# Kernel optimization log

Measured on AMD Instinct MI355X. Metric: run time of the kernel, lower is better.

## Reference

```python
import jax, jax.numpy as jnp
import numpy as np

CTX = 5  # context_len

def z_vector(x, ctx):
    # x: [B, L, E] -> [B, L, ctx*E]; slot j holds embedding of token (idx + j - ctx//2), zero-padded at edges
    half = ctx // 2
    B, L, E = x.shape
    xp = jnp.pad(x, ((0, 0), (half, half), (0, 0)))
    return jnp.concatenate([xp[:, i:i + L, :] for i in range(ctx)], axis=-1)

def setup_inputs() -> dict:
    key = jax.random.key(0)
    kq, ka, kw, kb = jax.random.split(key, 4)
    B, LQ, LA, E, F = 256, 64, 256, 300, 512
    question = jax.random.normal(kq, (B, LQ, E), dtype=jnp.float32)
    answer = jax.random.normal(ka, (B, LA, E), dtype=jnp.float32)
    W = jax.random.normal(kw, (CTX * E, F), dtype=jnp.float32) * 0.02
    b = jax.random.normal(kb, (F,), dtype=jnp.float32) * 0.02
    return {"question": question, "answer": answer, "W": W, "b": b}

def reference(question, answer, W, b):
    # Conv2d(1, F, (ctx*E, 1)) over the full-height Z vector == per-position linear map
    def branch(x):
        z = z_vector(x, CTX)                       # [B, L, ctx*E]
        out = jnp.einsum('blk,kf->bfl', z, W)      # [B, F, L]
        return out + b[None, :, None]
    return branch(question), branch(answer)
```

## Files before the change

### kernel.cpp

```cpp
#include <hip/hip_runtime.h>

#define NB   256
#define E0   300
#define EP   304
#define F_   512
#define KP   1536
#define NKT  48
#define LQ_  64
#define LA_  256

typedef __attribute__((ext_vector_type(4))) float f32x4;
typedef __attribute__((ext_vector_type(8))) short short8;

#define XQ_ELEMS (NB * (LQ_ + 4) * EP)
#define XA_ELEMS (NB * (LA_ + 4) * EP)
#define WF_ELEMS (F_ * KP)
#define OUTQ_ELEMS ((size_t)NB * F_ * LQ_)
#define XROWS (NB * (LQ_ + 4) + NB * (LA_ + 4))

__device__ __forceinline__ unsigned short f2bf(float x) {
    unsigned int u = __float_as_uint(x);
    u = u + 0x7fffu + ((u >> 16) & 1u);
    return (unsigned short)(u >> 16);
}

__global__ void prep_x(const float* __restrict__ q, const float* __restrict__ a,
                       unsigned short* __restrict__ xq, unsigned short* __restrict__ xa)
{
    int idx = blockIdx.x * 256 + threadIdx.x;
    if (idx >= XROWS * 76) return;
    int row = idx / 76;
    int col = idx - row * 76;

    const float* src;
    unsigned short* dst;
    bool valid;
    if (row < NB * (LQ_ + 4)) {
        int b = row / (LQ_ + 4), lp = row - b * (LQ_ + 4);
        dst = xq + (size_t)row * EP;
        valid = (lp >= 2 && lp < 2 + LQ_);
        src = q + ((size_t)b * LQ_ + (lp - 2)) * E0;
    } else {
        int r2 = row - NB * (LQ_ + 4);
        int b = r2 / (LA_ + 4), lp = r2 - b * (LA_ + 4);
        dst = xa + (size_t)r2 * EP;
        valid = (lp >= 2 && lp < 2 + LA_);
        src = a + ((size_t)b * LA_ + (lp - 2)) * E0;
    }
    unsigned long long pk = 0ull;
    if (valid && col < 75) {
        const float4 v = reinterpret_cast<const float4*>(src)[col];
        pk = (unsigned long long)f2bf(v.x)
           | ((unsigned long long)f2bf(v.y) << 16)
           | ((unsigned long long)f2bf(v.z) << 32)
           | ((unsigned long long)f2bf(v.w) << 48);
    }
    *reinterpret_cast<unsigned long long*>(dst + (size_t)col * 4) = pk;
}

__global__ void prep_w2(const float* __restrict__ W, unsigned short* __restrict__ wfr)
{
    int idx = blockIdx.x * 256 + threadIdx.x;
    int j    = idx & 7;
    int lane = (idx >> 3) & 63;
    int chunk = idx >> 9;
    int kc = chunk % NKT;
    int tile16 = chunk / NKT;
    int f  = tile16 * 16 + (lane & 15);
    int kp = kc * 32 + (lane >> 4) * 8 + j;
    int jj = kp / EP;
    int e  = kp - jj * EP;
    float v = (kp < 5 * EP && e < E0) ? W[(size_t)(jj * E0 + e) * F_ + f] : 0.f;
    wfr[idx] = f2bf(v);
}

__global__ __launch_bounds__(256, 3) void qa_gemm(
    const unsigned short* __restrict__ xq,
    const unsigned short* __restrict__ xa,
    const unsigned short* __restrict__ wfr,
    const float* __restrict__ bias,
    float* __restrict__ out)
{
    __shared__ __align__(16) unsigned short lds[4 * 2048];

    const int bid = blockIdx.x;
    const int wg  = (bid & 7) * 320 + (bid >> 3);

    const unsigned short* xp;
    float* ob;
    int Mbase, lsh, Lp, ftBase;
    if (wg < 512) {
        Mbase  = (wg >> 1) * 64;
        ftBase = (wg & 1) * 256;
        xp = xq; lsh = 6; Lp = LQ_ + 4;
        ob = out;
    } else {
        const int id = wg - 512;
        Mbase  = (id >> 1) * 64;
        ftBase = (id & 1) * 256;
        xp = xa; lsh = 8; Lp = LA_ + 4;
        ob = out + OUTQ_ELEMS;
    }
    const int Lv = 1 << lsh;

    const int tid  = threadIdx.x;
    const int lane = tid & 63;
    const int wid  = tid >> 6;
    const int lq   = lane >> 4;
    const int lr   = lane & 15;

    const int s_c  = (lane & 3) ^ ((lane >> 3) & 3);
    const int sub  = lane >> 2;
    const int mr0 = Mbase + wid * 16 + sub;
    const unsigned short* gZ0 = xp + (size_t)((mr0 >> lsh) * Lp + (mr0 & (Lv - 1))) * EP + s_c * 8;
    const int dz0 = wid * 512;

#define GLLDS(p, d) __builtin_amdgcn_global_load_lds(                               \
        (const __attribute__((address_space(1))) void*)(p),                         \
        (__attribute__((address_space(3))) void*)(d), 16, 0, 0)
#define STAGE_Z(T) do { const int rb = ((T) & 3) * 2048; const size_t ko = (size_t)(T) * 32; \
    GLLDS(gZ0 + ko, lds + dz0 + rb); } while (0)

    const unsigned short* wpc0 = wfr + (size_t)((ftBase >> 4) + wid * 4 + 0) * NKT * 512 + lane * 8;
    const unsigned short* wpc1 = wfr + (size_t)((ftBase >> 4) + wid * 4 + 1) * NKT * 512 + lane * 8;
    const unsigned short* wpc2 = wfr + (size_t)((ftBase >> 4) + wid * 4 + 2) * NKT * 512 + lane * 8;
    const unsigned short* wpc3 = wfr + (size_t)((ftBase >> 4) + wid * 4 + 3) * NKT * 512 + lane * 8;

#define WLOAD(dst, p) do {                                                           \
    asm volatile("global_load_dwordx4 %0, %1, off" : "=v"(dst) : "v"(p) : "memory"); \
    (p) += 512; } while (0)

    const int cs = (lq ^ ((lr >> 1) & 3)) * 16;
    int zoff[4];
#pragma unroll
    for (int n = 0; n < 4; ++n) zoff[n] = (n * 16 + lr) * 64 + cs;

    f32x4 acc[4][4] = {};
    short8 WA0, WA1, WA2, WA3, WB0, WB1, WB2, WB3;

#define MFMA(a, b, c) __builtin_amdgcn_mfma_f32_16x16x32_bf16((a), (b), (c), 0, 0, 0)

#define KSTEP(T, C0, C1, C2, C3, N0, N1, N2, N3, DO_W, DO_Z, AV) do {               \
    const char* bb = (const char*)lds + ((T) & 3) * 4096;                           \
    short8 zf[4];                                                                   \
    _Pragma("unroll") for (int n = 0; n < 4; ++n) zf[n] = *(const short8*)(bb + zoff[n]); \
    if (DO_W) { WLOAD(N0, wpc0); WLOAD(N1, wpc1); WLOAD(N2, wpc2); WLOAD(N3, wpc3); } \
    if (DO_Z) { STAGE_Z((T) + 3); }                                                 \
    asm volatile("s_waitcnt vmcnt(" #AV ") lgkmcnt(0)" ::: "memory");               \
    __builtin_amdgcn_sched_barrier(0);                                              \
    _Pragma("unroll") for (int n = 0; n < 4; ++n) {                                 \
        acc[0][n] = MFMA(C0, zf[n], acc[0][n]);                                     \
        acc[1][n] = MFMA(C1, zf[n], acc[1][n]);                                     \
        acc[2][n] = MFMA(C2, zf[n], acc[2][n]);                                     \
        acc[3][n] = MFMA(C3, zf[n], acc[3][n]);                                     \
    }                                                                               \
    asm volatile("s_barrier" ::: "memory");                                         \
} while (0)

    WLOAD(WA0, wpc0); WLOAD(WA1, wpc1); WLOAD(WA2, wpc2); WLOAD(WA3, wpc3);
    STAGE_Z(0); STAGE_Z(1); STAGE_Z(2);
    asm volatile("s_waitcnt vmcnt(2)\n\ts_barrier" ::: "memory");

    for (int i = 0; i < 22; ++i) {
        const int t = 2 * i;
        KSTEP(t,     WA0, WA1, WA2, WA3, WB0, WB1, WB2, WB3, 1, 1, 6);
        KSTEP(t + 1, WB0, WB1, WB2, WB3, WA0, WA1, WA2, WA3, 1, 1, 6);
    }
    KSTEP(44, WA0, WA1, WA2, WA3, WB0, WB1, WB2, WB3, 1, 1, 6);
    KSTEP(45, WB0, WB1, WB2, WB3, WA0, WA1, WA2, WA3, 1, 0, 5);
    KSTEP(46, WA0, WA1, WA2, WA3, WB0, WB1, WB2, WB3, 1, 0, 4);
    KSTEP(47, WB0, WB1, WB2, WB3, WA0, WA1, WA2, WA3, 0, 0, 0);

#undef KSTEP
#undef WLOAD
#undef STAGE_Z
#undef GLLDS
#undef MFMA

#pragma unroll
    for (int ns = 0; ns < 4; ++ns) {
        const int m = Mbase + ns * 16 + lr;
        const int b = m >> lsh;
        const int l = m & (Lv - 1);
        float* orow = ob + ((size_t)b * F_ << lsh) + l;
#pragma unroll
        for (int ms = 0; ms < 4; ++ms) {
            const int f0 = ftBase + wid * 64 + ms * 16 + lq * 4;
            const f32x4 v = acc[ms][ns];
#pragma unroll
            for (int r = 0; r < 4; ++r)
                orow[(size_t)(f0 + r) << lsh] = v[r] + __ldg(&bias[f0 + r]);
        }
    }
}

extern "C" void kernel_launch(void* const* d_in, const int* in_sizes, int n_in,
                              void* d_out, int out_size, void* d_ws, size_t ws_size,
                              hipStream_t stream)
{
    const float* q    = (const float*)d_in[0];
    const float* a    = (const float*)d_in[1];
    const float* W    = (const float*)d_in[2];
    const float* bias = (const float*)d_in[3];
    float* out = (float*)d_out;

    unsigned short* xq  = (unsigned short*)d_ws;
    unsigned short* xa  = xq + XQ_ELEMS;
    unsigned short* wfr = xa + XA_ELEMS;

    prep_x<<<(XROWS * 76 + 255) / 256, 256, 0, stream>>>(q, a, xq, xa);
    prep_w2<<<WF_ELEMS / 256, 256, 0, stream>>>(W, wfr);
    qa_gemm<<<2560, 256, 0, stream>>>(xq, xa, wfr, bias, out);
}
```

Baseline: 169.0 us.

## Stage Z in 128-wide superstages with double buffering and register prefetch

Replaces the 4-deep per-k-step LDS ring (one barrier per 32-wide k-step) with a 2-buffer scheme. Each stage loads four k-steps of Z at once, so there is one barrier per 128 k. LDS fragments for the next sub-step are prefetched into registers while the MFMAs for the current one issue, and s_setprio raises wave priority around the MFMA blocks. The aim is fewer workgroup barriers and better overlap of LDS reads with matrix math. The cost is a doubled LDS footprint (32KB), which may reduce occupancy, and more registers.

```diff
diff --git a/kernel.cpp b/kernel.cpp
--- a/kernel.cpp
+++ b/kernel.cpp
@@ -6,6 +6,7 @@
 #define F_   512
 #define KP   1536
 #define NKT  48
+#define NSS  12
 #define LQ_  64
 #define LA_  256
 
@@ -81,7 +82,7 @@
     const float* __restrict__ bias,
     float* __restrict__ out)
 {
-    __shared__ __align__(16) unsigned short lds[4 * 2048];
+    __shared__ __align__(16) unsigned short lds[2 * 8192];
 
     const int bid = blockIdx.x;
     const int wg  = (bid & 7) * 320 + (bid >> 3);
@@ -118,8 +119,11 @@
 #define GLLDS(p, d) __builtin_amdgcn_global_load_lds(                               \
         (const __attribute__((address_space(1))) void*)(p),                         \
         (__attribute__((address_space(3))) void*)(d), 16, 0, 0)
-#define STAGE_Z(T) do { const int rb = ((T) & 3) * 2048; const size_t ko = (size_t)(T) * 32; \
-    GLLDS(gZ0 + ko, lds + dz0 + rb); } while (0)
+#define STAGE_SS(T) do { const int rb = ((T) & 1) * 8192; const size_t ko = (size_t)(T) * 128; \
+    GLLDS(gZ0 + ko +  0, lds + rb + 0 * 2048 + dz0);                                \
+    GLLDS(gZ0 + ko + 32, lds + rb + 1 * 2048 + dz0);                                \
+    GLLDS(gZ0 + ko + 64, lds + rb + 2 * 2048 + dz0);                                \
+    GLLDS(gZ0 + ko + 96, lds + rb + 3 * 2048 + dz0); } while (0)
 
     const unsigned short* wpc0 = wfr + (size_t)((ftBase >> 4) + wid * 4 + 0) * NKT * 512 + lane * 8;
     const unsigned short* wpc1 = wfr + (size_t)((ftBase >> 4) + wid * 4 + 1) * NKT * 512 + lane * 8;
@@ -136,44 +140,56 @@
     for (int n = 0; n < 4; ++n) zoff[n] = (n * 16 + lr) * 64 + cs;
 
     f32x4 acc[4][4] = {};
-    short8 WA0, WA1, WA2, WA3, WB0, WB1, WB2, WB3;
+    short8 zA[4], zB[4], wA[4], wB[4];
 
 #define MFMA(a, b, c) __builtin_amdgcn_mfma_f32_16x16x32_bf16((a), (b), (c), 0, 0, 0)
 
-#define KSTEP(T, C0, C1, C2, C3, N0, N1, N2, N3, DO_W, DO_Z, AV) do {               \
-    const char* bb = (const char*)lds + ((T) & 3) * 4096;                           \
-    short8 zf[4];                                                                   \
-    _Pragma("unroll") for (int n = 0; n < 4; ++n) zf[n] = *(const short8*)(bb + zoff[n]); \
-    if (DO_W) { WLOAD(N0, wpc0); WLOAD(N1, wpc1); WLOAD(N2, wpc2); WLOAD(N3, wpc3); } \
-    if (DO_Z) { STAGE_Z((T) + 3); }                                                 \
-    asm volatile("s_waitcnt vmcnt(" #AV ") lgkmcnt(0)" ::: "memory");               \
+#define KSUB(bb, NXT, ZU, ZL, WU, WL, DO_ZRD, DO_W, VMCV, LGKV) do {                \
+    if (DO_ZRD) { _Pragma("unroll") for (int n = 0; n < 4; ++n)                     \
+        ZL[n] = *(const short8*)((bb) + (NXT) * 4096 + zoff[n]); }                  \
+    if (DO_W) { WLOAD(WL[0], wpc0); WLOAD(WL[1], wpc1);                             \
+                WLOAD(WL[2], wpc2); WLOAD(WL[3], wpc3); }                           \
+    asm volatile("s_waitcnt vmcnt(" #VMCV ") lgkmcnt(" #LGKV ")" ::: "memory");     \
     __builtin_amdgcn_sched_barrier(0);                                              \
+    __builtin_amdgcn_s_setprio(1);                                                  \
     _Pragma("unroll") for (int n = 0; n < 4; ++n) {                                 \
-        acc[0][n] = MFMA(C0, zf[n], acc[0][n]);                                     \
-        acc[1][n] = MFMA(C1, zf[n], acc[1][n]);                                     \
-        acc[2][n] = MFMA(C2, zf[n], acc[2][n]);                                     \
-        acc[3][n] = MFMA(C3, zf[n], acc[3][n]);                                     \
+        acc[0][n] = MFMA(WU[0], ZU[n], acc[0][n]);                                  \
+        acc[1][n] = MFMA(WU[1], ZU[n], acc[1][n]);                                  \
+        acc[2][n] = MFMA(WU[2], ZU[n], acc[2][n]);                                  \
+        acc[3][n] = MFMA(WU[3], ZU[n], acc[3][n]);                                  \
     }                                                                               \
-    asm volatile("s_barrier" ::: "memory");                                         \
+    __builtin_amdgcn_s_setprio(0);                                                  \
+    __builtin_amdgcn_sched_barrier(0);                                              \
 } while (0)
 
-    WLOAD(WA0, wpc0); WLOAD(WA1, wpc1); WLOAD(WA2, wpc2); WLOAD(WA3, wpc3);
-    STAGE_Z(0); STAGE_Z(1); STAGE_Z(2);
-    asm volatile("s_waitcnt vmcnt(2)\n\ts_barrier" ::: "memory");
-
-    for (int i = 0; i < 22; ++i) {
-        const int t = 2 * i;
-        KSTEP(t,     WA0, WA1, WA2, WA3, WB0, WB1, WB2, WB3, 1, 1, 6);
-        KSTEP(t + 1, WB0, WB1, WB2, WB3, WA0, WA1, WA2, WA3, 1, 1, 6);
-    }
-    KSTEP(44, WA0, WA1, WA2, WA3, WB0, WB1, WB2, WB3, 1, 1, 6);
-    KSTEP(45, WB0, WB1, WB2, WB3, WA0, WA1, WA2, WA3, 1, 0, 5);
-    KSTEP(46, WA0, WA1, WA2, WA3, WB0, WB1, WB2, WB3, 1, 0, 4);
-    KSTEP(47, WB0, WB1, WB2, WB3, WA0, WA1, WA2, WA3, 0, 0, 0);
-
-#undef KSTEP
+    WLOAD(wA[0], wpc0); WLOAD(wA[1], wpc1); WLOAD(wA[2], wpc2); WLOAD(wA[3], wpc3);
+    STAGE_SS(0);
+    asm volatile("s_waitcnt vmcnt(0)\n\ts_barrier" ::: "memory");
+
+    for (int S = 0; S < 11; ++S) {
+        const char* bb = (const char*)lds + (S & 1) * 16384;
+#pragma unroll
+        for (int n = 0; n < 4; ++n) zA[n] = *(const short8*)(bb + zoff[n]);
+        STAGE_SS(S + 1);
+        KSUB(bb, 1, zA, zB, wA, wB, 1, 1, 8, 4);
+        KSUB(bb, 2, zB, zA, wB, wA, 1, 1, 4, 4);
+        KSUB(bb, 3, zA, zB, wA, wB, 1, 1, 4, 4);
+        KSUB(bb, 0, zB, zA, wB, wA, 0, 1, 4, 0);
+        asm volatile("s_barrier" ::: "memory");
+    }
+    {
+        const char* bb = (const char*)lds + (11 & 1) * 16384;
+#pragma unroll
+        for (int n = 0; n < 4; ++n) zA[n] = *(const short8*)(bb + zoff[n]);
+        KSUB(bb, 1, zA, zB, wA, wB, 1, 1, 4, 4);
+        KSUB(bb, 2, zB, zA, wB, wA, 1, 1, 4, 4);
+        KSUB(bb, 3, zA, zB, wA, wB, 1, 1, 4, 4);
+        KSUB(bb, 0, zB, zA, wB, wA, 0, 0, 0, 0);
+    }
+
+#undef KSUB
 #undef WLOAD
-#undef STAGE_Z
+#undef STAGE_SS
 #undef GLLDS
 #undef MFMA
 
```

Result: faster. 164.1 us (-2.9%).

## Restructure GEMM pipeline into 4-step superstages with triple-buffered W registers

Applied to the files above, without the earlier changes.

Replaces the per-K-step LDS ring (4 slots of one 32-wide K chunk each, one barrier per step) with 3 LDS superstage buffers holding four K chunks each. This cuts workgroup barriers to one per four K steps, and the W fragments move to a three-deep register rotation. MFMA bursts are wrapped in s_setprio to favour matrix issue. LDS use grows from 16KB to 48KB per block, which may limit occupancy under launch_bounds(256,3), and the hand-tuned vmcnt values must exactly match the load order.

```diff
diff --git a/kernel.cpp b/kernel.cpp
--- a/kernel.cpp
+++ b/kernel.cpp
@@ -81,7 +81,7 @@
     const float* __restrict__ bias,
     float* __restrict__ out)
 {
-    __shared__ __align__(16) unsigned short lds[4 * 2048];
+    __shared__ __align__(16) unsigned short lds[3 * 8192];
 
     const int bid = blockIdx.x;
     const int wg  = (bid & 7) * 320 + (bid >> 3);
@@ -118,8 +118,11 @@
 #define GLLDS(p, d) __builtin_amdgcn_global_load_lds(                               \
         (const __attribute__((address_space(1))) void*)(p),                         \
         (__attribute__((address_space(3))) void*)(d), 16, 0, 0)
-#define STAGE_Z(T) do { const int rb = ((T) & 3) * 2048; const size_t ko = (size_t)(T) * 32; \
-    GLLDS(gZ0 + ko, lds + dz0 + rb); } while (0)
+#define STAGE_SS(T, RB3) do { const int rb = (RB3) * 8192; const size_t ko = (size_t)(T) * 128; \
+    GLLDS(gZ0 + ko +  0, lds + rb + 0 * 2048 + dz0);                                \
+    GLLDS(gZ0 + ko + 32, lds + rb + 1 * 2048 + dz0);                                \
+    GLLDS(gZ0 + ko + 64, lds + rb + 2 * 2048 + dz0);                                \
+    GLLDS(gZ0 + ko + 96, lds + rb + 3 * 2048 + dz0); } while (0)
 
     const unsigned short* wpc0 = wfr + (size_t)((ftBase >> 4) + wid * 4 + 0) * NKT * 512 + lane * 8;
     const unsigned short* wpc1 = wfr + (size_t)((ftBase >> 4) + wid * 4 + 1) * NKT * 512 + lane * 8;
@@ -129,6 +132,8 @@
 #define WLOAD(dst, p) do {                                                           \
     asm volatile("global_load_dwordx4 %0, %1, off" : "=v"(dst) : "v"(p) : "memory"); \
     (p) += 512; } while (0)
+#define WLD4(G) do { WLOAD(G[0], wpc0); WLOAD(G[1], wpc1);                           \
+                     WLOAD(G[2], wpc2); WLOAD(G[3], wpc3); } while (0)
 
     const int cs = (lq ^ ((lr >> 1) & 3)) * 16;
     int zoff[4];
@@ -136,44 +141,60 @@
     for (int n = 0; n < 4; ++n) zoff[n] = (n * 16 + lr) * 64 + cs;
 
     f32x4 acc[4][4] = {};
-    short8 WA0, WA1, WA2, WA3, WB0, WB1, WB2, WB3;
+    short8 w0[4], w1[4], w2[4];
 
 #define MFMA(a, b, c) __builtin_amdgcn_mfma_f32_16x16x32_bf16((a), (b), (c), 0, 0, 0)
 
-#define KSTEP(T, C0, C1, C2, C3, N0, N1, N2, N3, DO_W, DO_Z, AV) do {               \
-    const char* bb = (const char*)lds + ((T) & 3) * 4096;                           \
-    short8 zf[4];                                                                   \
-    _Pragma("unroll") for (int n = 0; n < 4; ++n) zf[n] = *(const short8*)(bb + zoff[n]); \
-    if (DO_W) { WLOAD(N0, wpc0); WLOAD(N1, wpc1); WLOAD(N2, wpc2); WLOAD(N3, wpc3); } \
-    if (DO_Z) { STAGE_Z((T) + 3); }                                                 \
-    asm volatile("s_waitcnt vmcnt(" #AV ") lgkmcnt(0)" ::: "memory");               \
-    __builtin_amdgcn_sched_barrier(0);                                              \
-    _Pragma("unroll") for (int n = 0; n < 4; ++n) {                                 \
-        acc[0][n] = MFMA(C0, zf[n], acc[0][n]);                                     \
-        acc[1][n] = MFMA(C1, zf[n], acc[1][n]);                                     \
-        acc[2][n] = MFMA(C2, zf[n], acc[2][n]);                                     \
-        acc[3][n] = MFMA(C3, zf[n], acc[3][n]);                                     \
-    }                                                                               \
-    asm volatile("s_barrier" ::: "memory");                                         \
-} while (0)
-
-    WLOAD(WA0, wpc0); WLOAD(WA1, wpc1); WLOAD(WA2, wpc2); WLOAD(WA3, wpc3);
-    STAGE_Z(0); STAGE_Z(1); STAGE_Z(2);
-    asm volatile("s_waitcnt vmcnt(2)\n\ts_barrier" ::: "memory");
-
-    for (int i = 0; i < 22; ++i) {
-        const int t = 2 * i;
-        KSTEP(t,     WA0, WA1, WA2, WA3, WB0, WB1, WB2, WB3, 1, 1, 6);
-        KSTEP(t + 1, WB0, WB1, WB2, WB3, WA0, WA1, WA2, WA3, 1, 1, 6);
-    }
-    KSTEP(44, WA0, WA1, WA2, WA3, WB0, WB1, WB2, WB3, 1, 1, 6);
-    KSTEP(45, WB0, WB1, WB2, WB3, WA0, WA1, WA2, WA3, 1, 0, 5);
-    KSTEP(46, WA0, WA1, WA2, WA3, WB0, WB1, WB2, WB3, 1, 0, 4);
-    KSTEP(47, WB0, WB1, WB2, WB3, WA0, WA1, WA2, WA3, 0, 0, 0);
-
-#undef KSTEP
+#define FENCE(VM, LG) do {                                                           \
+    asm volatile("s_waitcnt vmcnt(" #VM ") lgkmcnt(" #LG ")" ::: "memory");          \
+    __builtin_amdgcn_sched_barrier(0); } while (0)
+
+#define MFMA16(WU, ZU) do {                                                          \
+    __builtin_amdgcn_s_setprio(1);                                                   \
+    _Pragma("unroll") for (int n = 0; n < 4; ++n) {                                  \
+        acc[0][n] = MFMA(WU[0], ZU[n], acc[0][n]);                                   \
+        acc[1][n] = MFMA(WU[1], ZU[n], acc[1][n]);                                   \
+        acc[2][n] = MFMA(WU[2], ZU[n], acc[2][n]);                                   \
+        acc[3][n] = MFMA(WU[3], ZU[n], acc[3][n]);                                   \
+    }                                                                                \
+    __builtin_amdgcn_s_setprio(0);                                                   \
+    __builtin_amdgcn_sched_barrier(0); } while (0)
+
+#define ZRD(DST, BLK) do { _Pragma("unroll") for (int n = 0; n < 4; ++n)             \
+    DST[n] = *(const short8*)(bb + (BLK) * 4096 + zoff[n]); } while (0)
+
+#define SSBODY(P, WA_, WB_, WC_, DO_ST, STT, STB, DW2, DW3, V0, V1, V2, V3)          \
+{   const char* bb = (const char*)lds + (P) * 16384;                                 \
+    short8 zA[4], zB[4];                                                             \
+    ZRD(zA, 0);                                                                      \
+     ZRD(zB, 1); WLD4(WC_);                  FENCE(V0, 4); MFMA16(WA_, zA); \
+     ZRD(zA, 2); WLD4(WA_);                  FENCE(V1, 4); MFMA16(WB_, zB); \
+     ZRD(zB, 3); if (DW2) { WLD4(WB_); }                                    \
+              if (DO_ST) { STAGE_SS(STT, STB); }      FENCE(V2, 4); MFMA16(WC_, zA); \
+     if (DW3) { WLD4(WC_); }                 FENCE(V3, 0); MFMA16(WA_, zB); \
+    asm volatile("s_barrier" ::: "memory");                                          \
+}
+
+    WLD4(w0); WLD4(w1);
+    STAGE_SS(0, 0); STAGE_SS(1, 1);
+    asm volatile("s_waitcnt vmcnt(0)\n\ts_barrier" ::: "memory");
+
+    for (int Sb = 0; Sb < 9; Sb += 3) {
+        SSBODY(0, w0, w1, w2, 1, Sb + 2, 2, 1, 1, 12, 8, 12, 12);
+        SSBODY(1, w1, w2, w0, 1, Sb + 3, 0, 1, 1, 12, 8, 12, 12);
+        SSBODY(2, w2, w0, w1, 1, Sb + 4, 1, 1, 1, 12, 8, 12, 12);
+    }
+    SSBODY(0, w0, w1, w2, 1, 11, 2, 1, 1, 12, 8, 12, 12);
+    SSBODY(1, w1, w2, w0, 0, 0, 0, 1, 1, 12, 8, 8, 8);
+    SSBODY(2, w2, w0, w1, 0, 0, 0, 0, 0, 8, 8, 4, 0);
+
+#undef SSBODY
+#undef ZRD
+#undef MFMA16
+#undef FENCE
+#undef WLD4
 #undef WLOAD
-#undef STAGE_Z
+#undef STAGE_SS
 #undef GLLDS
 #undef MFMA
 
```

New measurement: 162.4 us. -3.9%, faster.

## Switch GEMM to 32x32x16 MFMA with 128x128 tiles and triple-buffered LDS

Applied to the files above, without the earlier changes.

Reworks the main GEMM from 16x16x32 MFMAs on 64-row by 256-feature tiles to 32x32x16 MFMAs on 128-row by 128-feature tiles. W is repacked into a 32-wide fragment layout, Z is staged 64 K-elements per step into a rotating three-buffer LDS ring, and MFMA bursts are wrapped in s_setprio. The aim is fewer LDS reads per MFMA, better operand reuse, and fewer pipeline barriers. In exchange the kernel uses 48KB of LDS and more accumulator registers, which may lower occupancy.

```diff
diff --git a/kernel.cpp b/kernel.cpp
--- a/kernel.cpp
+++ b/kernel.cpp
@@ -5,12 +5,11 @@
 #define EP   304
 #define F_   512
 #define KP   1536
-#define NKT  48
 #define LQ_  64
 #define LA_  256
 
-typedef __attribute__((ext_vector_type(4))) float f32x4;
-typedef __attribute__((ext_vector_type(8))) short short8;
+typedef __attribute__((ext_vector_type(16))) float f32x16;
+typedef __attribute__((ext_vector_type(8)))  short short8;
 
 #define XQ_ELEMS (NB * (LQ_ + 4) * EP)
 #define XA_ELEMS (NB * (LA_ + 4) * EP)
@@ -58,16 +57,16 @@
     *reinterpret_cast<unsigned long long*>(dst + (size_t)col * 4) = pk;
 }
 
-__global__ void prep_w2(const float* __restrict__ W, unsigned short* __restrict__ wfr)
+__global__ void prep_w3(const float* __restrict__ W, unsigned short* __restrict__ wfr)
 {
     int idx = blockIdx.x * 256 + threadIdx.x;
     int j    = idx & 7;
     int lane = (idx >> 3) & 63;
-    int chunk = idx >> 9;
-    int kc = chunk % NKT;
-    int tile16 = chunk / NKT;
-    int f  = tile16 * 16 + (lane & 15);
-    int kp = kc * 32 + (lane >> 4) * 8 + j;
+    int rem  = idx >> 9;
+    int kf   = rem % 96;
+    int t32  = rem / 96;
+    int f  = t32 * 32 + (lane & 31);
+    int kp = kf * 16 + (lane >> 5) * 8 + j;
     int jj = kp / EP;
     int e  = kp - jj * EP;
     float v = (kp < 5 * EP && e < E0) ? W[(size_t)(jj * E0 + e) * F_ + f] : 0.f;
@@ -81,23 +80,23 @@
     const float* __restrict__ bias,
     float* __restrict__ out)
 {
-    __shared__ __align__(16) unsigned short lds[4 * 2048];
+    __shared__ __align__(16) unsigned short lds[3 * 8192];
 
     const int bid = blockIdx.x;
     const int wg  = (bid & 7) * 320 + (bid >> 3);
 
+    const int ftq = wg / 640;
+    const int lt  = wg - ftq * 640;
+
     const unsigned short* xp;
     float* ob;
-    int Mbase, lsh, Lp, ftBase;
-    if (wg < 512) {
-        Mbase  = (wg >> 1) * 64;
-        ftBase = (wg & 1) * 256;
+    int Mbase, lsh, Lp;
+    if (lt < 128) {
+        Mbase = lt * 128;
         xp = xq; lsh = 6; Lp = LQ_ + 4;
         ob = out;
     } else {
-        const int id = wg - 512;
-        Mbase  = (id >> 1) * 64;
-        ftBase = (id & 1) * 256;
+        Mbase = (lt - 128) * 128;
         xp = xa; lsh = 8; Lp = LA_ + 4;
         ob = out + OUTQ_ELEMS;
     }
@@ -106,90 +105,105 @@
     const int tid  = threadIdx.x;
     const int lane = tid & 63;
     const int wid  = tid >> 6;
-    const int lq   = lane >> 4;
-    const int lr   = lane & 15;
+    const int l31  = lane & 31;
+    const int lhi  = lane >> 5;
 
     const int s_c  = (lane & 3) ^ ((lane >> 3) & 3);
     const int sub  = lane >> 2;
-    const int mr0 = Mbase + wid * 16 + sub;
-    const unsigned short* gZ0 = xp + (size_t)((mr0 >> lsh) * Lp + (mr0 & (Lv - 1))) * EP + s_c * 8;
-    const int dz0 = wid * 512;
+    const int mrA = Mbase + wid * 32 + sub;
+    const int mrB = mrA + 16;
+    const unsigned short* gZ0 = xp + (size_t)((mrA >> lsh) * Lp + (mrA & (Lv - 1))) * EP + s_c * 8;
+    const unsigned short* gZ1 = xp + (size_t)((mrB >> lsh) * Lp + (mrB & (Lv - 1))) * EP + s_c * 8;
+    const int dzA = wid * 1024;
+    const int dzB = dzA + 512;
 
 #define GLLDS(p, d) __builtin_amdgcn_global_load_lds(                               \
         (const __attribute__((address_space(1))) void*)(p),                         \
         (__attribute__((address_space(3))) void*)(d), 16, 0, 0)
-#define STAGE_Z(T) do { const int rb = ((T) & 3) * 2048; const size_t ko = (size_t)(T) * 32; \
-    GLLDS(gZ0 + ko, lds + dz0 + rb); } while (0)
-
-    const unsigned short* wpc0 = wfr + (size_t)((ftBase >> 4) + wid * 4 + 0) * NKT * 512 + lane * 8;
-    const unsigned short* wpc1 = wfr + (size_t)((ftBase >> 4) + wid * 4 + 1) * NKT * 512 + lane * 8;
-    const unsigned short* wpc2 = wfr + (size_t)((ftBase >> 4) + wid * 4 + 2) * NKT * 512 + lane * 8;
-    const unsigned short* wpc3 = wfr + (size_t)((ftBase >> 4) + wid * 4 + 3) * NKT * 512 + lane * 8;
+#define ST4(RB, T) do { const size_t ko = (size_t)(T) * 64;                         \
+    GLLDS(gZ0 + ko,      lds + (RB) + dzA);                                         \
+    GLLDS(gZ1 + ko,      lds + (RB) + dzB);                                         \
+    GLLDS(gZ0 + ko + 32, lds + (RB) + 4096 + dzA);                                  \
+    GLLDS(gZ1 + ko + 32, lds + (RB) + 4096 + dzB); } while (0)
+
+    const unsigned short* wp = wfr + (size_t)(ftq * 4 + wid) * (96 * 512) + lane * 8;
 
 #define WLOAD(dst, p) do {                                                           \
     asm volatile("global_load_dwordx4 %0, %1, off" : "=v"(dst) : "v"(p) : "memory"); \
     (p) += 512; } while (0)
-
-    const int cs = (lq ^ ((lr >> 1) & 3)) * 16;
-    int zoff[4];
-#pragma unroll
-    for (int n = 0; n < 4; ++n) zoff[n] = (n * 16 + lr) * 64 + cs;
-
-    f32x4 acc[4][4] = {};
-    short8 WA0, WA1, WA2, WA3, WB0, WB1, WB2, WB3;
-
-#define MFMA(a, b, c) __builtin_amdgcn_mfma_f32_16x16x32_bf16((a), (b), (c), 0, 0, 0)
-
-#define KSTEP(T, C0, C1, C2, C3, N0, N1, N2, N3, DO_W, DO_Z, AV) do {               \
-    const char* bb = (const char*)lds + ((T) & 3) * 4096;                           \
-    short8 zf[4];                                                                   \
-    _Pragma("unroll") for (int n = 0; n < 4; ++n) zf[n] = *(const short8*)(bb + zoff[n]); \
-    if (DO_W) { WLOAD(N0, wpc0); WLOAD(N1, wpc1); WLOAD(N2, wpc2); WLOAD(N3, wpc3); } \
-    if (DO_Z) { STAGE_Z((T) + 3); }                                                 \
-    asm volatile("s_waitcnt vmcnt(" #AV ") lgkmcnt(0)" ::: "memory");               \
-    __builtin_amdgcn_sched_barrier(0);                                              \
-    _Pragma("unroll") for (int n = 0; n < 4; ++n) {                                 \
-        acc[0][n] = MFMA(C0, zf[n], acc[0][n]);                                     \
-        acc[1][n] = MFMA(C1, zf[n], acc[1][n]);                                     \
-        acc[2][n] = MFMA(C2, zf[n], acc[2][n]);                                     \
-        acc[3][n] = MFMA(C3, zf[n], acc[3][n]);                                     \
-    }                                                                               \
+#define W4(SET) do { WLOAD(SET[0], wp); WLOAD(SET[1], wp);                           \
+                     WLOAD(SET[2], wp); WLOAD(SET[3], wp); } while (0)
+
+    const int swr = (l31 >> 1) & 3;
+    int boff[4][2];
+#pragma unroll
+    for (int nt = 0; nt < 4; ++nt)
+#pragma unroll
+        for (int ks = 0; ks < 2; ++ks)
+            boff[nt][ks] = (nt * 32 + l31) * 64 + ((ks * 2 + lhi) ^ swr) * 16;
+
+    f32x16 acc[4] = {};
+    short8 wA[4], wB[4], bfr[4][2];
+
+#define MFMA32(a, b, c) __builtin_amdgcn_mfma_f32_32x32x16_bf16((a), (b), (c), 0, 0, 0)
+#define RDB(BB) do { _Pragma("unroll") for (int nt = 0; nt < 4; ++nt)               \
+    _Pragma("unroll") for (int ks = 0; ks < 2; ++ks)                                \
+        bfr[nt][ks] = *(const short8*)((BB) + boff[nt][ks]); } while (0)
+#define MFMA8(C, SET) do { _Pragma("unroll") for (int nt = 0; nt < 4; ++nt) {       \
+        acc[nt] = MFMA32(SET[2 * (C) + 0], bfr[nt][0], acc[nt]);                    \
+        acc[nt] = MFMA32(SET[2 * (C) + 1], bfr[nt][1], acc[nt]);                    \
+    } } while (0)
+#define SB __builtin_amdgcn_sched_barrier(0)
+#define SP1 __builtin_amdgcn_s_setprio(1)
+#define SP0 __builtin_amdgcn_s_setprio(0)
+
+    int rbPrev = 16384, rbCur = 0, rbNext = 8192;
+
+#define SS(SET, DO_ST, DO_W, TT, VM)                                                \
+{   if (DO_ST) ST4(rbPrev, TT);                                                     \
+    const char* bb = (const char*)(lds + rbCur);                                    \
+    RDB(bb);                                                                        \
+    asm volatile("s_waitcnt vmcnt(" #VM ") lgkmcnt(0)" ::: "memory"); SB;           \
+    SP1; MFMA8(0, SET); SP0; SB;                                                    \
+    RDB(bb + 8192);                                                                 \
+    asm volatile("s_waitcnt lgkmcnt(0)" ::: "memory"); SB;                          \
+    SP1; MFMA8(1, SET); SP0; SB;                                                    \
+    if (DO_W) W4(SET);                                                              \
     asm volatile("s_barrier" ::: "memory");                                         \
-} while (0)
-
-    WLOAD(WA0, wpc0); WLOAD(WA1, wpc1); WLOAD(WA2, wpc2); WLOAD(WA3, wpc3);
-    STAGE_Z(0); STAGE_Z(1); STAGE_Z(2);
-    asm volatile("s_waitcnt vmcnt(2)\n\ts_barrier" ::: "memory");
-
-    for (int i = 0; i < 22; ++i) {
-        const int t = 2 * i;
-        KSTEP(t,     WA0, WA1, WA2, WA3, WB0, WB1, WB2, WB3, 1, 1, 6);
-        KSTEP(t + 1, WB0, WB1, WB2, WB3, WA0, WA1, WA2, WA3, 1, 1, 6);
-    }
-    KSTEP(44, WA0, WA1, WA2, WA3, WB0, WB1, WB2, WB3, 1, 1, 6);
-    KSTEP(45, WB0, WB1, WB2, WB3, WA0, WA1, WA2, WA3, 1, 0, 5);
-    KSTEP(46, WA0, WA1, WA2, WA3, WB0, WB1, WB2, WB3, 1, 0, 4);
-    KSTEP(47, WB0, WB1, WB2, WB3, WA0, WA1, WA2, WA3, 0, 0, 0);
-
-#undef KSTEP
+    { int _t = rbPrev; rbPrev = rbCur; rbCur = rbNext; rbNext = _t; }               \
+}
+
+    W4(wA); ST4(0, 0); ST4(8192, 1); W4(wB);
+    asm volatile("s_waitcnt vmcnt(8)\n\ts_barrier" ::: "memory");
+
+    for (int S = 0; S < 22; S += 2) {
+        SS(wA, 1, 1, S + 2, 8);
+        SS(wB, 1, 1, S + 3, 8);
+    }
+    SS(wA, 0, 0, 0, 4);
+    SS(wB, 0, 0, 0, 0);
+
+#undef SS
+#undef MFMA8
+#undef RDB
+#undef MFMA32
+#undef W4
 #undef WLOAD
-#undef STAGE_Z
+#undef ST4
 #undef GLLDS
-#undef MFMA
-
-#pragma unroll
-    for (int ns = 0; ns < 4; ++ns) {
-        const int m = Mbase + ns * 16 + lr;
+
+    const int fwbase = ftq * 128 + wid * 32;
+#pragma unroll
+    for (int nt = 0; nt < 4; ++nt) {
+        const int m = Mbase + nt * 32 + l31;
         const int b = m >> lsh;
-        const int l = m & (Lv - 1);
-        float* orow = ob + ((size_t)b * F_ << lsh) + l;
-#pragma unroll
-        for (int ms = 0; ms < 4; ++ms) {
-            const int f0 = ftBase + wid * 64 + ms * 16 + lq * 4;
-            const f32x4 v = acc[ms][ns];
-#pragma unroll
-            for (int r = 0; r < 4; ++r)
-                orow[(size_t)(f0 + r) << lsh] = v[r] + __ldg(&bias[f0 + r]);
+        const int lcol = m & (Lv - 1);
+        float* orow = ob + ((size_t)b * F_ << lsh) + lcol;
+        const f32x16 v = acc[nt];
+#pragma unroll
+        for (int reg = 0; reg < 16; ++reg) {
+            const int f = fwbase + (reg & 3) + 8 * (reg >> 2) + 4 * lhi;
+            orow[(size_t)f << lsh] = v[reg] + __ldg(&bias[f]);
         }
     }
 }
@@ -209,6 +223,6 @@
     unsigned short* wfr = xa + XA_ELEMS;
 
     prep_x<<<(XROWS * 76 + 255) / 256, 256, 0, stream>>>(q, a, xq, xa);
-    prep_w2<<<WF_ELEMS / 256, 256, 0, stream>>>(W, wfr);
+    prep_w3<<<WF_ELEMS / 256, 256, 0, stream>>>(W, wfr);
     qa_gemm<<<2560, 256, 0, stream>>>(xq, xa, wfr, bias, out);
 }
```

New measurement: 212.4 us. 25.7% more time.
